# Kernel optimization log

Hardware: AMD Instinct MI355X
Metric: run time of the kernel (lower is better)

## Reference

```python
import jax, jax.numpy as jnp
import numpy as np

COS_EPS = 0.001
THRESHOLD = 0.1
LEAKY_SLOPE = 0.01


def setup_inputs() -> dict:
    key = jax.random.key(0)
    k1, k2 = jax.random.split(key)
    B, N, D_in, D_out = 4, 4096, 256, 128
    b_het_z = jax.random.normal(k1, (B, N, D_in), dtype=jnp.float32)
    # xavier_uniform with gain=1.414
    gain = 1.414
    bound = gain * np.sqrt(6.0 / (D_in + D_out))
    W = jax.random.uniform(k2, (D_in, D_out), dtype=jnp.float32, minval=-bound, maxval=bound)
    return {"b_het_z": b_het_z, "W": W}


def reference(b_het_z, W):
    # h: [B, N, D_out]
    h = jnp.matmul(b_het_z, W)
    h = jax.nn.leaky_relu(h, negative_slope=LEAKY_SLOPE)
    # pairwise cosine similarity via normalized GEMM (avoids O(N^2*D) broadcast)
    # torch CosineSimilarity: dot(x, y) / max(||x|| * ||y||, eps)
    norms = jnp.linalg.norm(h, axis=-1)  # [B, N]
    dots = jnp.einsum("bnd,bmd->bnm", h, h)  # [B, N, N]
    denom = jnp.maximum(norms[:, :, None] * norms[:, None, :], COS_EPS)
    b_adj = jnp.abs(dots / denom)
    # nn.Threshold(t, 0): keep x if x > t else 0
    b_adj = jnp.where(b_adj > THRESHOLD, b_adj, 0.0)
    return b_adj
```

## Files before the change

### kernel.cpp

```cpp
#include <hip/hip_runtime.h>
#include <math.h>

#define NTOK 4096
#define RTOT 16384
#define DIN  256
#define DOUT 128

constexpr float LEAKY = 0.01f;
constexpr float THR   = 0.1f;

typedef __attribute__((ext_vector_type(8)))  short bf16x8;
typedef __attribute__((ext_vector_type(16))) float f32x16;

__device__ __forceinline__ unsigned short f2bf(float x) {
    unsigned u = __float_as_uint(x);
    unsigned r = (u + 0x7fffu + ((u >> 16) & 1u)) >> 16;
    return (unsigned short)r;
}
__device__ __forceinline__ float bf2f(unsigned short h) {
    return __uint_as_float((unsigned)h << 16);
}

__device__ __forceinline__ void gload_lds16(const void* g, void* l) {
    __builtin_amdgcn_global_load_lds(
        (const __attribute__((address_space(1))) void*)g,
        (__attribute__((address_space(3))) void*)l,
        16, 0, 0);
}

__global__ __launch_bounds__(256, 2) void proj_kernel(
    const float* __restrict__ A, const float* __restrict__ W,
    unsigned short* __restrict__ Hhi, unsigned short* __restrict__ Hlo)
{
    __shared__ float As[32 * DIN];
    __shared__ float Ws[64 * DOUT];
    const int tid  = threadIdx.x;
    const int row0 = blockIdx.x * 32;

    {
        const float4* src = (const float4*)(A + (size_t)row0 * DIN);
        float4* dst = (float4*)As;
        #pragma unroll
        for (int it = 0; it < 8; ++it)
            dst[tid + it * 256] = src[tid + it * 256];
    }

    const int tx = tid & 31;
    const int ty = tid >> 5;

    float acc[4][4];
    #pragma unroll
    for (int i = 0; i < 4; ++i)
        #pragma unroll
        for (int j = 0; j < 4; ++j) acc[i][j] = 0.f;

    for (int kc = 0; kc < DIN; kc += 64) {
        __syncthreads();
        {
            const float4* wsrc = (const float4*)(W + (size_t)kc * DOUT);
            float4* wdst = (float4*)Ws;
            #pragma unroll
            for (int it = 0; it < 8; ++it)
                wdst[tid + it * 256] = wsrc[tid + it * 256];
        }
        __syncthreads();

        for (int k = 0; k < 64; k += 4) {
            float4 w4[4];
            #pragma unroll
            for (int s = 0; s < 4; ++s)
                w4[s] = *(const float4*)(Ws + (k + s) * DOUT + 4 * tx);
            #pragma unroll
            for (int i = 0; i < 4; ++i) {
                float4 a4 = *(const float4*)(As + (ty + 8 * i) * DIN + kc + k);
                float ak[4] = {a4.x, a4.y, a4.z, a4.w};
                #pragma unroll
                for (int s = 0; s < 4; ++s) {
                    float wj[4] = {w4[s].x, w4[s].y, w4[s].z, w4[s].w};
                    #pragma unroll
                    for (int j = 0; j < 4; ++j)
                        acc[i][j] = fmaf(ak[s], wj[j], acc[i][j]);
                }
            }
        }
    }

    #pragma unroll
    for (int i = 0; i < 4; ++i) {
        float h[4];
        float s = 0.f;
        #pragma unroll
        for (int j = 0; j < 4; ++j) {
            float v = acc[i][j];
            h[j] = (v >= 0.f) ? v : LEAKY * v;
            s = fmaf(h[j], h[j], s);
        }
        #pragma unroll
        for (int m = 16; m >= 1; m >>= 1)
            s += __shfl_xor(s, m, 64);
        const float rinv = 1.0f / sqrtf(s);
        const int r = row0 + ty + 8 * i;
        ushort4 hv, lv;
        {
            float n0 = h[0] * rinv; hv.x = f2bf(n0); lv.x = f2bf(n0 - bf2f(hv.x));
            float n1 = h[1] * rinv; hv.y = f2bf(n1); lv.y = f2bf(n1 - bf2f(hv.y));
            float n2 = h[2] * rinv; hv.z = f2bf(n2); lv.z = f2bf(n2 - bf2f(hv.z));
            float n3 = h[3] * rinv; hv.w = f2bf(n3); lv.w = f2bf(n3 - bf2f(hv.w));
        }
        *(ushort4*)(Hhi + (size_t)r * DOUT + 4 * tx) = hv;
        *(ushort4*)(Hlo + (size_t)r * DOUT + 4 * tx) = lv;
    }
}

__global__ __launch_bounds__(256, 4) void cos_kernel(
    const unsigned short* __restrict__ Hhi,
    const unsigned short* __restrict__ Hlo,
    float* __restrict__ out)
{
    __shared__ uint4 smem4[2048];
    char* smem = (char*)smem4;

    const int b  = blockIdx.y;
    const int ti = (blockIdx.x >> 5) << 7;
    const int tj = (blockIdx.x & 31) << 7;
    const int bN = b * NTOK;

    const int tid  = threadIdx.x;
    const int wave = tid >> 6;
    const int lane = tid & 63;
    const int qr = wave & 1;
    const int qc = wave >> 1;
    const int lr = lane & 31;
    const int hh = lane >> 5;

    const unsigned short* gbase =
        ((wave & 1) ? Hlo : Hhi)
        + (((size_t)(bN + ((wave >> 1) ? tj : ti) + (lane >> 2))) << 7)
        + ((size_t)(((lane & 3) ^ ((lane >> 2) & 3)) << 3));
    char* lbase = smem + (wave << 13);

    f32x16 acc[2][2];
    #pragma unroll
    for (int i = 0; i < 2; ++i)
        #pragma unroll
        for (int j = 0; j < 2; ++j)
            #pragma unroll
            for (int e = 0; e < 16; ++e)
                acc[i][j][e] = 0.f;

    for (int kc = 0; kc < DOUT; kc += 32) {
        __syncthreads();
        #pragma unroll
        for (int it = 0; it < 8; ++it)
            gload_lds16(gbase + kc + it * 2048, lbase + (it << 10));
        __syncthreads();

        #pragma unroll
        for (int ks = 0; ks < 2; ++ks) {
            bf16x8 ah[2], al[2], bh[2], bl[2];
            const int s = (ks << 1) | hh;
            #pragma unroll
            for (int t = 0; t < 2; ++t) {
                const int ra = qr * 64 + t * 32 + lr;
                const int oa = (ra << 6) + ((s ^ (ra & 3)) << 4);
                ah[t] = *(const bf16x8*)(smem + oa);
                al[t] = *(const bf16x8*)(smem + 8192 + oa);
                const int rb = qc * 64 + t * 32 + lr;
                const int ob = (rb << 6) + ((s ^ (rb & 3)) << 4);
                bh[t] = *(const bf16x8*)(smem + 16384 + ob);
                bl[t] = *(const bf16x8*)(smem + 24576 + ob);
            }
            #pragma unroll
            for (int i = 0; i < 2; ++i)
                #pragma unroll
                for (int j = 0; j < 2; ++j) {
                    acc[i][j] = __builtin_amdgcn_mfma_f32_32x32x16_bf16(
                                    ah[i], bh[j], acc[i][j], 0, 0, 0);
                    acc[i][j] = __builtin_amdgcn_mfma_f32_32x32x16_bf16(
                                    ah[i], bl[j], acc[i][j], 0, 0, 0);
                    acc[i][j] = __builtin_amdgcn_mfma_f32_32x32x16_bf16(
                                    al[i], bh[j], acc[i][j], 0, 0, 0);
                }
        }
    }

    float* Ob = out + (size_t)b * NTOK * NTOK;
    const int col = tj + qc * 64 + lr;
    #pragma unroll
    for (int i = 0; i < 2; ++i) {
        const int rbase = ti + qr * 64 + i * 32 + (hh << 2);
        #pragma unroll
        for (int j = 0; j < 2; ++j) {
            const int c = col + j * 32;
            #pragma unroll
            for (int v = 0; v < 16; ++v) {
                const int row = rbase + (v & 3) + ((v >> 2) << 3);
                float x = fabsf(acc[i][j][v]);
                x = (x > THR) ? x : 0.f;
                __builtin_nontemporal_store(x, Ob + (size_t)row * NTOK + c);
            }
        }
    }
}

extern "C" void kernel_launch(void* const* d_in, const int* in_sizes, int n_in,
                              void* d_out, int out_size, void* d_ws, size_t ws_size,
                              hipStream_t stream) {
    const float* A = (const float*)d_in[0];
    const float* W = (const float*)d_in[1];
    float* out = (float*)d_out;

    unsigned short* Hhi = (unsigned short*)d_ws;
    unsigned short* Hlo = Hhi + (size_t)RTOT * DOUT;

    proj_kernel<<<RTOT / 32, 256, 0, stream>>>(A, W, Hhi, Hlo);
    cos_kernel<<<dim3(1024, 4), 256, 0, stream>>>(Hhi, Hlo, out);
}
```

Baseline: 327.7 us.

## Double-buffer LDS K-chunks and stage epilogue through LDS for 16-byte stores

Replaces the single-buffered 32-wide K loop with eight 16-wide steps that are double-buffered in LDS. The global-to-LDS load for the next step is issued before the MFMAs of the current one, so load latency is hidden behind compute with one barrier per step. The epilogue now writes thresholded results into an LDS tile in two halves, then every thread reads them back and issues coalesced 16-byte nontemporal stores, instead of scattered 4-byte stores. This adds LDS traffic and extra barriers in the epilogue, and the new LDS layout has no XOR swizzle, so bank conflicts may rise.

```diff
diff --git a/kernel.cpp b/kernel.cpp
--- a/kernel.cpp
+++ b/kernel.cpp
@@ -11,6 +11,7 @@
 
 typedef __attribute__((ext_vector_type(8)))  short bf16x8;
 typedef __attribute__((ext_vector_type(16))) float f32x16;
+typedef __attribute__((ext_vector_type(4)))  float f32x4;
 
 __device__ __forceinline__ unsigned short f2bf(float x) {
     unsigned u = __float_as_uint(x);
@@ -117,8 +118,7 @@
     const unsigned short* __restrict__ Hlo,
     float* __restrict__ out)
 {
-    __shared__ uint4 smem4[2048];
-    char* smem = (char*)smem4;
+    __shared__ __align__(16) char smem[32768];
 
     const int b  = blockIdx.y;
     const int ti = (blockIdx.x >> 5) << 7;
@@ -133,11 +133,19 @@
     const int lr = lane & 31;
     const int hh = lane >> 5;
 
-    const unsigned short* gbase =
+    const unsigned short* gsrc =
         ((wave & 1) ? Hlo : Hhi)
-        + (((size_t)(bN + ((wave >> 1) ? tj : ti) + (lane >> 2))) << 7)
-        + ((size_t)(((lane & 3) ^ ((lane >> 2) & 3)) << 3));
-    char* lbase = smem + (wave << 13);
+        + (((size_t)(bN + ((wave >> 1) ? tj : ti)
+                     + ((lane >> 4) << 3) + (lane & 7))) << 7)
+        + (((lane >> 3) & 1) << 3);
+    const int lsec = wave << 12;
+
+    int offA[2], offB[2];
+    #pragma unroll
+    for (int t = 0; t < 2; ++t) {
+        offA[t] = (((qr * 8 + t * 4 + (lr >> 3)) << 8) | (hh << 7) | ((lr & 7) << 4));
+        offB[t] = (((qc * 8 + t * 4 + (lr >> 3)) << 8) | (hh << 7) | ((lr & 7) << 4));
+    }
 
     f32x16 acc[2][2];
     #pragma unroll
@@ -148,58 +156,76 @@
             for (int e = 0; e < 16; ++e)
                 acc[i][j][e] = 0.f;
 
-    for (int kc = 0; kc < DOUT; kc += 32) {
-        __syncthreads();
-        #pragma unroll
-        for (int it = 0; it < 8; ++it)
-            gload_lds16(gbase + kc + it * 2048, lbase + (it << 10));
-        __syncthreads();
-
-        #pragma unroll
-        for (int ks = 0; ks < 2; ++ks) {
-            bf16x8 ah[2], al[2], bh[2], bl[2];
-            const int s = (ks << 1) | hh;
-            #pragma unroll
-            for (int t = 0; t < 2; ++t) {
-                const int ra = qr * 64 + t * 32 + lr;
-                const int oa = (ra << 6) + ((s ^ (ra & 3)) << 4);
-                ah[t] = *(const bf16x8*)(smem + oa);
-                al[t] = *(const bf16x8*)(smem + 8192 + oa);
-                const int rb = qc * 64 + t * 32 + lr;
-                const int ob = (rb << 6) + ((s ^ (rb & 3)) << 4);
-                bh[t] = *(const bf16x8*)(smem + 16384 + ob);
-                bl[t] = *(const bf16x8*)(smem + 24576 + ob);
+    #pragma unroll
+    for (int it = 0; it < 4; ++it)
+        gload_lds16(gsrc + it * 32 * DOUT, smem + lsec + (it << 10));
+    __syncthreads();
+
+    int cur = 0;
+    #pragma unroll
+    for (int r = 0; r < 8; ++r) {
+        if (r < 7) {
+            const unsigned short* g = gsrc + (r + 1) * 16;
+            char* l = smem + ((cur ^ 1) << 14) + lsec;
+            #pragma unroll
+            for (int it = 0; it < 4; ++it)
+                gload_lds16(g + it * 32 * DOUT, l + (it << 10));
+        }
+
+        const char* base = smem + (cur << 14);
+        bf16x8 ah[2], al[2], bh[2], bl[2];
+        #pragma unroll
+        for (int t = 0; t < 2; ++t) {
+            ah[t] = *(const bf16x8*)(base +         offA[t]);
+            al[t] = *(const bf16x8*)(base +  4096 + offA[t]);
+            bh[t] = *(const bf16x8*)(base +  8192 + offB[t]);
+            bl[t] = *(const bf16x8*)(base + 12288 + offB[t]);
+        }
+        #pragma unroll
+        for (int i = 0; i < 2; ++i)
+            #pragma unroll
+            for (int j = 0; j < 2; ++j) {
+                acc[i][j] = __builtin_amdgcn_mfma_f32_32x32x16_bf16(
+                                ah[i], bh[j], acc[i][j], 0, 0, 0);
+                acc[i][j] = __builtin_amdgcn_mfma_f32_32x32x16_bf16(
+                                ah[i], bl[j], acc[i][j], 0, 0, 0);
+                acc[i][j] = __builtin_amdgcn_mfma_f32_32x32x16_bf16(
+                                al[i], bh[j], acc[i][j], 0, 0, 0);
             }
+        __syncthreads();
+        cur ^= 1;
+    }
+
+    float* Ob = out + (size_t)b * NTOK * NTOK;
+    float* T = (float*)smem;
+    #pragma unroll
+    for (int h = 0; h < 2; ++h) {
+        if (qr == h) {
             #pragma unroll
             for (int i = 0; i < 2; ++i)
                 #pragma unroll
                 for (int j = 0; j < 2; ++j) {
-                    acc[i][j] = __builtin_amdgcn_mfma_f32_32x32x16_bf16(
-                                    ah[i], bh[j], acc[i][j], 0, 0, 0);
-                    acc[i][j] = __builtin_amdgcn_mfma_f32_32x32x16_bf16(
-                                    ah[i], bl[j], acc[i][j], 0, 0, 0);
-                    acc[i][j] = __builtin_amdgcn_mfma_f32_32x32x16_bf16(
-                                    al[i], bh[j], acc[i][j], 0, 0, 0);
+                    const int c0 = qc * 64 + j * 32 + lr;
+                    #pragma unroll
+                    for (int v = 0; v < 16; ++v) {
+                        const int rt = i * 32 + (hh << 2) + (v & 3) + ((v >> 2) << 3);
+                        float x = fabsf(acc[i][j][v]);
+                        x = (x > THR) ? x : 0.f;
+                        T[(rt << 7) + c0] = x;
+                    }
                 }
         }
-    }
-
-    float* Ob = out + (size_t)b * NTOK * NTOK;
-    const int col = tj + qc * 64 + lr;
-    #pragma unroll
-    for (int i = 0; i < 2; ++i) {
-        const int rbase = ti + qr * 64 + i * 32 + (hh << 2);
-        #pragma unroll
-        for (int j = 0; j < 2; ++j) {
-            const int c = col + j * 32;
-            #pragma unroll
-            for (int v = 0; v < 16; ++v) {
-                const int row = rbase + (v & 3) + ((v >> 2) << 3);
-                float x = fabsf(acc[i][j][v]);
-                x = (x > THR) ? x : 0.f;
-                __builtin_nontemporal_store(x, Ob + (size_t)row * NTOK + c);
-            }
-        }
+        __syncthreads();
+        #pragma unroll
+        for (int it = 0; it < 8; ++it) {
+            const int idx = tid + it * 256;
+            const int rt  = idx >> 5;
+            const int c   = (idx & 31) << 2;
+            f32x4 v = *(const f32x4*)(T + (rt << 7) + c);
+            __builtin_nontemporal_store(
+                v, (f32x4*)(Ob + (size_t)(ti + h * 64 + rt) * NTOK + tj + c));
+        }
+        __syncthreads();
     }
 }
 
```

New measurement: 340.6 us. 1.04x slower.
